# Performance work log

Measured on AMD Instinct MI355X. Metric: run time of the kernel, lower is better.

Reference implementation:

```python
import jax, jax.numpy as jnp
import numpy as np

STEPS = 100
VTH = 1.0
POOL_TH = 0.75


def _conv(x, w):
    # 5x5 conv, stride 1, pad 2, no bias; NCHW / OIHW
    return jax.lax.conv_general_dilated(
        x, w, window_strides=(1, 1), padding=[(2, 2), (2, 2)],
        dimension_numbers=('NCHW', 'OIHW', 'NCHW'))


def _avgpool2(x):
    s = jax.lax.reduce_window(x, 0.0, jax.lax.add, (1, 1, 2, 2), (1, 1, 2, 2), 'VALID')
    return s * 0.25


def _fire(mem, th):
    # torch.nn.functional.threshold(mem, th, 0): keep values > th, else 0
    ex = jnp.where(mem > th, mem, 0.0)
    mem = mem - ex
    out = (ex > 0).astype(mem.dtype)
    return mem, out


def _ave(output, inp):
    c = inp >= output
    denom = jnp.sum(jnp.where(c, inp, 0.0))
    num = jnp.sum(jnp.where(c, output, 0.0))
    return jnp.where(denom < 1e-3, 1.0, num / denom)


def _ave_p(output, inp):
    denom = jnp.sum(inp)
    return jnp.where(denom < 1e-3, 1.0, jnp.sum(output) / denom)


def setup_inputs() -> dict:
    key = jax.random.key(0)
    k_in, k1, k2, k3, k4 = jax.random.split(key, 5)
    B = 512
    inputdata = jax.random.uniform(k_in, (B, 1, 28, 28), dtype=jnp.float32)
    w1 = jax.random.normal(k1, (20, 1, 5, 5), dtype=jnp.float32) * np.sqrt(2.0 / (5 * 5 * 1))
    w2 = jax.random.normal(k2, (50, 20, 5, 5), dtype=jnp.float32) * np.sqrt(2.0 / (5 * 5 * 20))
    wf0 = jax.random.normal(k3, (200, 2450), dtype=jnp.float32) * np.sqrt(2.0 / 2450)
    wf1 = jax.random.normal(k4, (10, 200), dtype=jnp.float32) * np.sqrt(2.0 / 200)
    return {'inputdata': inputdata, 'w1': w1, 'w2': w2, 'wf0': wf0, 'wf1': wf1}


def _spiking_loop(inputdata, w1, w2, wf0, wf1):
    B = inputdata.shape[0]
    f32 = jnp.float32
    z = lambda *s: jnp.zeros(s, f32)
    carry0 = (
        z(B, 20, 28, 28), z(B, 20, 14, 14), z(B, 50, 14, 14), z(B, 50, 7, 7), z(B, 200),  # membranes
        z(B, 1, 28, 28),                                                                   # Total_input
        z(B, 20, 28, 28), z(B, 20, 28, 28),   # Total_1_output, IF_in_c1
        z(B, 20, 14, 14), z(B, 20, 14, 14),   # Total_p1_output, IF_in_p1
        z(B, 50, 14, 14), z(B, 50, 14, 14),   # Total_2_output, IF_in_c2
        z(B, 50, 7, 7), z(B, 50, 7, 7),       # Total_p2_output, IF_in_p2
        z(B, 200), z(B, 200),                  # Total_f0_output, IF_in_f0
    )

    sgn = jnp.sign(inputdata)
    half = jnp.abs(inputdata) / 2.0

    def step(carry, k):
        (m1, m1s, m2, m2s, mf0, Tin, T1, IFc1, Tp1, IFp1, T2, IFc2, Tp2, IFp2, Tf0, IFf0) = carry
        r = jax.random.uniform(k, inputdata.shape, dtype=f32)
        poisson = (half > r).astype(f32) * sgn
        Tin = Tin + poisson

        a = _conv(poisson, w1)
        m1 = m1 + a
        m1, o = _fire(m1, VTH)            # LIF (l=1 -> membrane unchanged)
        IFc1 = IFc1 + a
        T1 = T1 + o

        a = _avgpool2(o)
        m1s = m1s + a
        m1s, o = _fire(m1s, POOL_TH)
        IFp1 = IFp1 + a
        Tp1 = Tp1 + o

        a = _conv(o, w2)
        m2 = m2 + a
        m2, o = _fire(m2, VTH)
        IFc2 = IFc2 + a
        T2 = T2 + o

        a = _avgpool2(o)
        m2s = m2s + a
        m2s, o = _fire(m2s, POOL_TH)
        IFp2 = IFp2 + a
        Tp2 = Tp2 + o

        a = o.reshape(B, -1) @ wf0.T
        mf0 = mf0 + a
        mf0, o = _fire(mf0, VTH)
        IFf0 = IFf0 + a
        Tf0 = Tf0 + o

        return (m1, m1s, m2, m2s, mf0, Tin, T1, IFc1, Tp1, IFp1, T2, IFc2, Tp2, IFp2, Tf0, IFf0), None

    keys = jax.random.split(jax.random.key(42), STEPS)
    carry, _ = jax.lax.scan(step, carry0, keys)
    return jax.lax.stop_gradient(carry)  # loop ran under torch.no_grad()


def _forward(inputdata, w1, w2, wf0, wf1):
    sg = jax.lax.stop_gradient
    (_, _, _, _, _, Tin, T1, IFc1, Tp1, IFp1, T2, IFc2, Tp2, IFp2, Tf0, IFf0) = \
        _spiking_loop(inputdata, w1, w2, wf0, wf1)

    # global scales start at 1, sign == 1 branch taken
    s1 = 0.6 * _ave(T1, IFc1) + 0.4
    s2 = 0.6 * _ave_p(Tp1, IFp1) + 0.4
    s3 = 0.6 * _ave(T2, IFc2) + 0.4
    s4 = 0.6 * _ave_p(Tp2, IFp2) + 0.4
    s5 = 0.6 * _ave(Tf0, IFf0) + 0.4
    sc1 = s1 * (IFc1 > 0).astype(jnp.float32)
    sc2 = s2 * (IFp1 > 0).astype(jnp.float32)
    sc3 = s3 * (IFc2 > 0).astype(jnp.float32)
    sc4 = s4 * (IFp2 > 0).astype(jnp.float32)
    sc5 = s5 * (IFf0 > 0).astype(jnp.float32)

    # straight-through graph (ASF-BP)
    B = inputdata.shape[0]
    o = _conv(Tin, w1) * sc1
    T1g = o - sg(o) + T1
    o = _avgpool2(T1g) * sc2
    Tp1g = o - sg(o) + Tp1
    o = _conv(Tp1g, w2) * sc3
    T2g = o - sg(o) + T2
    o = _avgpool2(T2g) * sc4
    Tp2g = o - sg(o) + Tp2
    o = (Tp2g.reshape(B, -1) @ wf0.T) * sc5
    Tf0g = o - sg(o) + Tf0
    fc1_in = Tf0g @ wf1.T
    return fc1_in / VTH / STEPS


def reference(inputdata, w1, w2, wf0, wf1):
    return _forward(inputdata, w1, w2, wf0, wf1)
```

## Files before the change

kernel.cpp:

```cpp
#include <hip/hip_runtime.h>
#include <stdint.h>

#define STEPS 100

typedef float f2 __attribute__((ext_vector_type(2)));

__device__ __forceinline__ uint32_t rotl32(uint32_t v, int r) {
  return (v << r) | (v >> (32 - r));
}

__device__ __forceinline__ void tf2x32(uint32_t k0, uint32_t k1,
                                       uint32_t x0, uint32_t x1,
                                       uint32_t& o0, uint32_t& o1) {
  uint32_t ks2 = k0 ^ k1 ^ 0x1BD11BDAu;
  x0 += k0; x1 += k1;
#define RND(r) { x0 += x1; x1 = rotl32(x1, (r)); x1 ^= x0; }
  RND(13) RND(15) RND(26) RND(6)
  x0 += k1;  x1 += ks2 + 1u;
  RND(17) RND(29) RND(16) RND(24)
  x0 += ks2; x1 += k0 + 2u;
  RND(13) RND(15) RND(26) RND(6)
  x0 += k0;  x1 += k1 + 3u;
  RND(17) RND(29) RND(16) RND(24)
  x0 += k1;  x1 += ks2 + 4u;
  RND(13) RND(15) RND(26) RND(6)
  x0 += ks2; x1 += k0 + 5u;
#undef RND
  o0 = x0; o1 = x1;
}

__global__ void keys_k(uint32_t* __restrict__ kb) {
  int i = threadIdx.x;
  if (i < STEPS) {
    uint32_t a, b;
    tf2x32(0u, 42u, 0u, (uint32_t)i, a, b);
    kb[2 * i] = a;
    kb[2 * i + 1] = b;
  }
}

__global__ void wt3_k(const float* __restrict__ w2, float* __restrict__ wT3) {
  int i = blockIdx.x * blockDim.x + threadIdx.x;
  if (i >= 50 * 20 * 72) return;
  int oc = i / 1440, r = i % 1440;
  int ic = r / 72, q = r % 72;
  int jr = q / 12, p = q % 12;
  float v = 0.f;
  if (p < 10) {
    int kx = p >> 1, h = p & 1;
    if (h == 0 && jr < 5)  v = w2[oc * 500 + ic * 25 + jr * 5 + kx];
    if (h == 1 && jr >= 1) v = w2[oc * 500 + ic * 25 + (jr - 1) * 5 + kx];
  }
  wT3[i] = v;
}

__global__ void wf0t_k(const float* __restrict__ wf0,
                       float* __restrict__ wf0T) {
  int i = blockIdx.x * blockDim.x + threadIdx.x;
  if (i >= 2450 * 256) return;
  int k = i >> 8, n = i & 255;
  wf0T[i] = (n < 200) ? wf0[n * 2450 + k] : 0.f;
}

__device__ __forceinline__ void p2blk(const float4& q0, const float4& q1,
                                      const float4& q2, const float4& q3,
                                      const f2* wp, f2* acc2) {
  float u[18] = {q0.x, q0.y, q0.z, q0.w, q1.x, q1.y, q1.z, q1.w,
                 q2.x, q2.y, q2.z, q2.w, q3.x, q3.y, q3.z, q3.w, 0.f, 0.f};
#pragma unroll
  for (int kx = 0; kx < 5; ++kx) {
    f2 w = wp[kx];
#pragma unroll
    for (int xx = 0; xx < 14; ++xx) {
      f2 us = {u[xx + kx], u[xx + kx]};
      acc2[xx] = __builtin_elementwise_fma(w, us, acc2[xx]);
    }
  }
}

__device__ __forceinline__ void ldwp(const float* wic, int jr, f2* wp) {
  const float4* p = reinterpret_cast<const float4*>(wic + jr * 12);
  float4 a = p[0], b = p[1];
  float2 c = *reinterpret_cast<const float2*>(wic + jr * 12 + 8);
  wp[0] = f2{a.x, a.y}; wp[1] = f2{a.z, a.w};
  wp[2] = f2{b.x, b.y}; wp[3] = f2{b.z, b.w};
  wp[4] = f2{c.x, c.y};
}

__global__ __launch_bounds__(512, 2) void step_all_k(
    const float* __restrict__ x, const float* __restrict__ w1,
    const float* __restrict__ wT3, const uint32_t* __restrict__ kb,
    uint32_t* __restrict__ sp2g) {
  __shared__ __align__(16) float  xhs_l[784];
  __shared__ __align__(16) float  pois_l[32 * 34];
  __shared__ __align__(16) float  sp1_l[20 * 18 * 20];
  __shared__ int8_t s2_l[50 * 196];
  __shared__ __align__(16) float  m2_l[50 * 196];
  __shared__ float  m2s_l[2450];
  __shared__ float  m1s_l[20 * 196];
  __shared__ float  m1stash[512 * 21];

  const int b  = blockIdx.x;
  const int t  = threadIdx.x;
  const int lq = t & 255;
  const int ohu = __builtin_amdgcn_readfirstlane(t >> 8);
  const bool act1 = lq < 196;
  const int qy = lq / 14, qx = lq % 14;
  const bool act2 = t < 350;
  const int oc2 = t / 7;
  const int rp  = t % 7;
  const int y0  = 2 * rp;

  for (int p = t; p < 784; p += 512) {
    xhs_l[p] = x[b * 784 + p] * 0.5f;
  }
  for (int i = t; i < 32 * 34; i += 512) pois_l[i] = 0.f;
  for (int i = t; i < 20 * 360; i += 512) sp1_l[i] = 0.f;
  for (int i = t; i < 50 * 196; i += 512) m2_l[i] = 0.f;
  for (int i = t; i < 2450; i += 512) m2s_l[i] = 0.f;
  for (int i = t; i < 20 * 196; i += 512) m1s_l[i] = 0.f;
  for (int i = t; i < 512 * 21; i += 512) m1stash[i] = 0.f;

  float m1p[2][10];
#pragma unroll
  for (int i = 0; i < 10; ++i) {
    m1p[0][i] = 0.f;
    m1p[1][i] = 0.f;
  }
  __syncthreads();

  {
    uint32_t k0 = kb[0], k1 = kb[1];
    for (int p = t; p < 784; p += 512) {
      uint32_t o0, o1;
      tf2x32(k0, k1, 0u, (uint32_t)(b * 784 + p), o0, o1);
      float r = __uint_as_float(((o0 ^ o1) >> 9) | 0x3F800000u) - 1.0f;
      float v = xhs_l[p];
      pois_l[(p / 28 + 2) * 34 + (p % 28 + 2)] =
          (fabsf(v) > r) ? ((v > 0.f) ? 1.f : -1.f) : 0.f;
    }
  }
  __syncthreads();

#define LDROW(rr, d) {                                                      \
    const float2* _pr = reinterpret_cast<const float2*>(                    \
        &pois_l[(2 * qy + (rr)) * 34 + 2 * qx]);                            \
    float2 _a0 = _pr[0], _a1 = _pr[1], _a2 = _pr[2];                        \
    d[0] = _a0.x; d[1] = _a0.y; d[2] = _a1.x;                               \
    d[3] = _a1.y; d[4] = _a2.x; d[5] = _a2.y; }

#define LD4(base, p0, p1, p2, p3) {                                         \
    const float4* _rn = reinterpret_cast<const float4*>(base);              \
    p0 = _rn[0]; p1 = _rn[1]; p2 = _rn[2]; p3 = _rn[3]; }

  for (int s = 0; s < STEPS; ++s) {
    if (act1) {
      float rA[6], rB[6];
      LDROW(0, rA)
      LDROW(1, rB)
      float acc[4][10];
#pragma unroll
      for (int tt = 0; tt < 4; ++tt)
#pragma unroll
        for (int i = 0; i < 10; ++i) acc[tt][i] = 0.f;
#pragma unroll
      for (int ky = 0; ky < 5; ++ky) {
#pragma unroll
        for (int kx = 0; kx < 5; ++kx) {
#pragma unroll
          for (int i = 0; i < 10; ++i) {
            float w = w1[(ohu * 10 + i) * 25 + ky * 5 + kx];
            acc[0][i] += w * rA[kx];
            acc[1][i] += w * rA[kx + 1];
            acc[2][i] += w * rB[kx];
            acc[3][i] += w * rB[kx + 1];
          }
        }
        if (ky < 4) {
#pragma unroll
          for (int j = 0; j < 6; ++j) rA[j] = rB[j];
          LDROW(ky + 2, rB)
        }
      }
#pragma unroll
      for (int i = 0; i < 10; ++i) {
        float s4[4];
#pragma unroll
        for (int tt = 0; tt < 2; ++tt) {
          float m = m1p[tt][i] + acc[tt][i];
          float sp = 0.f;
          if (m > 1.0f) { sp = 1.f; m = 0.f; }
          m1p[tt][i] = m;
          s4[tt] = sp;
        }
        {
          float m = m1stash[t * 21 + i] + acc[2][i];
          float sp = 0.f;
          if (m > 1.0f) { sp = 1.f; m = 0.f; }
          m1stash[t * 21 + i] = m;
          s4[2] = sp;
        }
        {
          float m = m1stash[t * 21 + 10 + i] + acc[3][i];
          float sp = 0.f;
          if (m > 1.0f) { sp = 1.f; m = 0.f; }
          m1stash[t * 21 + 10 + i] = m;
          s4[3] = sp;
        }
        float a = 0.25f * (((s4[0] + s4[1]) + s4[2]) + s4[3]);
        int mi = (ohu * 10 + i) * 196 + lq;
        float mm = m1s_l[mi] + a;
        float spp = 0.f;
        if (mm > 0.75f) { spp = 1.f; mm = 0.f; }
        m1s_l[mi] = mm;
        sp1_l[(ohu * 10 + i) * 360 + (qy + 2) * 20 + (qx + 2)] = spp;
      }
    }
    __syncthreads();

    if (act2) {
      f2 acc2[14];
#pragma unroll
      for (int xx = 0; xx < 14; ++xx) acc2[xx] = f2{0.f, 0.f};
      const float* wb = wT3 + oc2 * 1440;
#pragma unroll 1
      for (int ic = 0; ic < 20; ++ic) {
        const float* wic = wb + ic * 72;
        const float* spi = sp1_l + ic * 360;
        float4 a0, a1, a2, a3, b0, b1, b2, b3;
        f2 wpA[5], wpB[5];
        LD4(spi + (y0 + 0) * 20, a0, a1, a2, a3)
        ldwp(wic, 0, wpA);
        LD4(spi + (y0 + 1) * 20, b0, b1, b2, b3)
        ldwp(wic, 1, wpB);
        p2blk(a0, a1, a2, a3, wpA, acc2);
        LD4(spi + (y0 + 2) * 20, a0, a1, a2, a3)
        ldwp(wic, 2, wpA);
        __builtin_amdgcn_sched_barrier(0);
        p2blk(b0, b1, b2, b3, wpB, acc2);
        LD4(spi + (y0 + 3) * 20, b0, b1, b2, b3)
        ldwp(wic, 3, wpB);
        __builtin_amdgcn_sched_barrier(0);
        p2blk(a0, a1, a2, a3, wpA, acc2);
        LD4(spi + (y0 + 4) * 20, a0, a1, a2, a3)
        ldwp(wic, 4, wpA);
        __builtin_amdgcn_sched_barrier(0);
        p2blk(b0, b1, b2, b3, wpB, acc2);
        LD4(spi + (y0 + 5) * 20, b0, b1, b2, b3)
        ldwp(wic, 5, wpB);
        __builtin_amdgcn_sched_barrier(0);
        p2blk(a0, a1, a2, a3, wpA, acc2);
        p2blk(b0, b1, b2, b3, wpB, acc2);
      }
#pragma unroll
      for (int xx = 0; xx < 14; ++xx) {
        int li = oc2 * 196 + y0 * 14 + xx;
        float m = m2_l[li] + acc2[xx].x;
        int8_t sp = 0;
        if (m > 1.0f) { sp = 1; m = 0.f; }
        m2_l[li] = m;
        s2_l[li] = sp;
      }
#pragma unroll
      for (int xx = 0; xx < 14; ++xx) {
        int li = oc2 * 196 + (y0 + 1) * 14 + xx;
        float m = m2_l[li] + acc2[xx].y;
        int8_t sp = 0;
        if (m > 1.0f) { sp = 1; m = 0.f; }
        m2_l[li] = m;
        s2_l[li] = sp;
      }
    }
    __syncthreads();

#pragma unroll
    for (int i = 0; i < 5; ++i) {
      int e = i * 512 + t;
      bool fire = false;
      if (e < 2450) {
        int oc = e / 49, qq = e % 49;
        int yo = qq / 7, xo = qq % 7;
        int ib = oc * 196 + 2 * yo * 14 + 2 * xo;
        float s00 = (float)s2_l[ib];
        float s01 = (float)s2_l[ib + 1];
        float s10 = (float)s2_l[ib + 14];
        float s11 = (float)s2_l[ib + 15];
        float a = 0.25f * (((s00 + s01) + s10) + s11);
        float m = m2s_l[e] + a;
        if (m > 0.75f) { fire = true; m = 0.f; }
        m2s_l[e] = m;
      }
      unsigned long long mask = __ballot(fire);
      int base = (e & ~63);
      if ((t & 63) == 0 && base < 2450) {
        int d = base >> 5;
        sp2g[b * 7700 + s * 77 + d] = (uint32_t)mask;
        if (base + 32 < 2450)
          sp2g[b * 7700 + s * 77 + d + 1] = (uint32_t)(mask >> 32);
      }
    }
    if (s + 1 < STEPS) {
      uint32_t k0 = kb[2 * (s + 1)], k1 = kb[2 * (s + 1) + 1];
      for (int p = t; p < 784; p += 512) {
        uint32_t o0, o1;
        tf2x32(k0, k1, 0u, (uint32_t)(b * 784 + p), o0, o1);
        float r = __uint_as_float(((o0 ^ o1) >> 9) | 0x3F800000u) - 1.0f;
        float v = xhs_l[p];
        pois_l[(p / 28 + 2) * 34 + (p % 28 + 2)] =
            (fabsf(v) > r) ? ((v > 0.f) ? 1.f : -1.f) : 0.f;
      }
    }
    __syncthreads();
  }
#undef LDROW
#undef LD4
}

__global__ __launch_bounds__(256) void fc0f_k(
    const uint32_t* __restrict__ sp2g, const float* __restrict__ wf0T,
    float* __restrict__ Tf0g) {
  __shared__ uint32_t mk[77];
  const int b = blockIdx.x;
  const int n = threadIdx.x;
  float m = 0.f, T = 0.f;
  for (int s = 0; s < STEPS; ++s) {
    __syncthreads();
    if (n < 77) mk[n] = sp2g[b * 7700 + s * 77 + n];
    __syncthreads();
    float acc = 0.f;
    for (int d = 0; d < 77; ++d) {
      uint32_t um = mk[d];
      while (um) {
        int j = __builtin_ctz(um);
        um &= um - 1;
        acc += wf0T[((d << 5) + j) * 256 + n];
      }
    }
    m += acc;
    if (m > 1.0f) { T += 1.f; m = 0.f; }
  }
  if (n < 200) Tf0g[b * 200 + n] = T;
}

__global__ void fc1_k(const float* __restrict__ Tf0,
                      const float* __restrict__ wf1,
                      float* __restrict__ out) {
  int idx = blockIdx.x * blockDim.x + threadIdx.x;
  if (idx >= 5120) return;
  int b = idx / 10, i = idx % 10;
  float a = 0.f;
  for (int j = 0; j < 200; ++j) a += Tf0[b * 200 + j] * wf1[i * 200 + j];
  out[idx] = (a / 1.0f) / 100.0f;
}

extern "C" void kernel_launch(void* const* d_in, const int* in_sizes, int n_in,
                              void* d_out, int out_size, void* d_ws, size_t ws_size,
                              hipStream_t stream) {
  (void)in_sizes; (void)n_in; (void)out_size; (void)ws_size;
  const float* x   = (const float*)d_in[0];
  const float* w1  = (const float*)d_in[1];
  const float* w2  = (const float*)d_in[2];
  const float* wf0 = (const float*)d_in[3];
  const float* wf1 = (const float*)d_in[4];
  float* out = (float*)d_out;
  char* ws = (char*)d_ws;

  const size_t tf0_b  = 512ull * 200 * 4;
  const size_t wt_b   = 50ull * 20 * 72 * 4;
  const size_t key_b  = 1024;
  const size_t wf0t_b = 2450ull * 256 * 4;
  float*    Tf0g = (float*)ws;
  float*    wT3  = (float*)(ws + tf0_b);
  uint32_t* kb   = (uint32_t*)(ws + tf0_b + wt_b);
  float*    wf0T = (float*)(ws + tf0_b + wt_b + key_b);
  uint32_t* sp2g = (uint32_t*)(ws + tf0_b + wt_b + key_b + wf0t_b);

  keys_k<<<1, 128, 0, stream>>>(kb);
  wt3_k<<<282, 256, 0, stream>>>(w2, wT3);
  wf0t_k<<<2450, 256, 0, stream>>>(wf0, wf0T);
  step_all_k<<<512, 512, 0, stream>>>(x, w1, wT3, kb, sp2g);
  fc0f_k<<<512, 256, 0, stream>>>(sp2g, wf0T, Tf0g);
  fc1_k<<<20, 256, 0, stream>>>(Tf0g, wf1, out);
}
```

Measured before the change: 10.38 ms.

## Fuse pool2 into conv2 threads, pipeline conv2 loads, overlap RNG on idle threads

Each conv2 thread now average-pools its own 2x14 output strip into the second pooled membrane and packs the 7 spike bits into a shared byte. This removes the int8 spike buffer, the separate pooling pass, and one block-wide barrier per step. Threads 0-76 then gather those bytes into 32-bit words for the global spike mask. The conv2 input-channel loop is software-pipelined, prefetching rows and weights for the next channel across iterations. Poisson generation for the next step moves onto the otherwise idle threads 384-511 so it overlaps with conv2, at the cost of fewer threads doing that RNG work and more complex bit-packing logic.

```diff
diff --git a/kernel.cpp b/kernel.cpp
--- a/kernel.cpp
+++ b/kernel.cpp
@@ -81,9 +81,9 @@
 __device__ __forceinline__ void ldwp(const float* wic, int jr, f2* wp) {
   const float4* p = reinterpret_cast<const float4*>(wic + jr * 12);
   float4 a = p[0], b = p[1];
-  float2 c = *reinterpret_cast<const float2*>(wic + jr * 12 + 8);
   wp[0] = f2{a.x, a.y}; wp[1] = f2{a.z, a.w};
   wp[2] = f2{b.x, b.y}; wp[3] = f2{b.z, b.w};
+  float2 c = *reinterpret_cast<const float2*>(wic + jr * 12 + 8);
   wp[4] = f2{c.x, c.y};
 }
 
@@ -94,11 +94,11 @@
   __shared__ __align__(16) float  xhs_l[784];
   __shared__ __align__(16) float  pois_l[32 * 34];
   __shared__ __align__(16) float  sp1_l[20 * 18 * 20];
-  __shared__ int8_t s2_l[50 * 196];
   __shared__ __align__(16) float  m2_l[50 * 196];
-  __shared__ float  m2s_l[2450];
-  __shared__ float  m1s_l[20 * 196];
-  __shared__ float  m1stash[512 * 21];
+  __shared__ float    m2s_l[2450];
+  __shared__ float    m1s_l[20 * 196];
+  __shared__ float    m1stash[512 * 21];
+  __shared__ uint8_t  fb[352];
 
   const int b  = blockIdx.x;
   const int t  = threadIdx.x;
@@ -120,6 +120,7 @@
   for (int i = t; i < 2450; i += 512) m2s_l[i] = 0.f;
   for (int i = t; i < 20 * 196; i += 512) m1s_l[i] = 0.f;
   for (int i = t; i < 512 * 21; i += 512) m1stash[i] = 0.f;
+  if (t < 352) fb[t] = 0;
 
   float m1p[2][10];
 #pragma unroll
@@ -149,8 +150,9 @@
     d[0] = _a0.x; d[1] = _a0.y; d[2] = _a1.x;                               \
     d[3] = _a1.y; d[4] = _a2.x; d[5] = _a2.y; }
 
-#define LD4(base, p0, p1, p2, p3) {                                         \
-    const float4* _rn = reinterpret_cast<const float4*>(base);              \
+#define LD4(icv, jrv, p0, p1, p2, p3) {                                     \
+    const float4* _rn = reinterpret_cast<const float4*>(                    \
+        sp1_l + (icv) * 360 + (y0 + (jrv)) * 20);                           \
     p0 = _rn[0]; p1 = _rn[1]; p2 = _rn[2]; p3 = _rn[3]; }
 
   for (int s = 0; s < STEPS; ++s) {
@@ -223,94 +225,101 @@
 #pragma unroll
       for (int xx = 0; xx < 14; ++xx) acc2[xx] = f2{0.f, 0.f};
       const float* wb = wT3 + oc2 * 1440;
+      float4 A0, A1, A2, A3, B0, B1, B2, B3;
+      f2 W0[5], W1[5], W2[5];
+      LD4(0, 0, A0, A1, A2, A3)
+      ldwp(wb, 0, W0);
+      LD4(0, 1, B0, B1, B2, B3)
+      ldwp(wb, 1, W1);
+      ldwp(wb, 2, W2);
 #pragma unroll 1
       for (int ic = 0; ic < 20; ++ic) {
-        const float* wic = wb + ic * 72;
-        const float* spi = sp1_l + ic * 360;
-        float4 a0, a1, a2, a3, b0, b1, b2, b3;
-        f2 wpA[5], wpB[5];
-        LD4(spi + (y0 + 0) * 20, a0, a1, a2, a3)
-        ldwp(wic, 0, wpA);
-        LD4(spi + (y0 + 1) * 20, b0, b1, b2, b3)
-        ldwp(wic, 1, wpB);
-        p2blk(a0, a1, a2, a3, wpA, acc2);
-        LD4(spi + (y0 + 2) * 20, a0, a1, a2, a3)
-        ldwp(wic, 2, wpA);
-        __builtin_amdgcn_sched_barrier(0);
-        p2blk(b0, b1, b2, b3, wpB, acc2);
-        LD4(spi + (y0 + 3) * 20, b0, b1, b2, b3)
-        ldwp(wic, 3, wpB);
-        __builtin_amdgcn_sched_barrier(0);
-        p2blk(a0, a1, a2, a3, wpA, acc2);
-        LD4(spi + (y0 + 4) * 20, a0, a1, a2, a3)
-        ldwp(wic, 4, wpA);
-        __builtin_amdgcn_sched_barrier(0);
-        p2blk(b0, b1, b2, b3, wpB, acc2);
-        LD4(spi + (y0 + 5) * 20, b0, b1, b2, b3)
-        ldwp(wic, 5, wpB);
-        __builtin_amdgcn_sched_barrier(0);
-        p2blk(a0, a1, a2, a3, wpA, acc2);
-        p2blk(b0, b1, b2, b3, wpB, acc2);
-      }
+        const int icn = (ic < 19) ? ic + 1 : 19;
+        const float* wic  = wb + ic * 72;
+        const float* wicn = wb + icn * 72;
+        p2blk(A0, A1, A2, A3, W0, acc2);
+        LD4(ic, 2, A0, A1, A2, A3)
+        ldwp(wic, 3, W0);
+        __builtin_amdgcn_sched_barrier(0);
+        p2blk(B0, B1, B2, B3, W1, acc2);
+        LD4(ic, 3, B0, B1, B2, B3)
+        ldwp(wic, 4, W1);
+        __builtin_amdgcn_sched_barrier(0);
+        p2blk(A0, A1, A2, A3, W2, acc2);
+        LD4(ic, 4, A0, A1, A2, A3)
+        ldwp(wic, 5, W2);
+        __builtin_amdgcn_sched_barrier(0);
+        p2blk(B0, B1, B2, B3, W0, acc2);
+        LD4(ic, 5, B0, B1, B2, B3)
+        ldwp(wicn, 0, W0);
+        __builtin_amdgcn_sched_barrier(0);
+        p2blk(A0, A1, A2, A3, W1, acc2);
+        LD4(icn, 0, A0, A1, A2, A3)
+        ldwp(wicn, 1, W1);
+        __builtin_amdgcn_sched_barrier(0);
+        p2blk(B0, B1, B2, B3, W2, acc2);
+        LD4(icn, 1, B0, B1, B2, B3)
+        ldwp(wicn, 2, W2);
+        __builtin_amdgcn_sched_barrier(0);
+      }
+      float f0[14], f1[14];
 #pragma unroll
       for (int xx = 0; xx < 14; ++xx) {
         int li = oc2 * 196 + y0 * 14 + xx;
         float m = m2_l[li] + acc2[xx].x;
-        int8_t sp = 0;
-        if (m > 1.0f) { sp = 1; m = 0.f; }
+        float sp = 0.f;
+        if (m > 1.0f) { sp = 1.f; m = 0.f; }
         m2_l[li] = m;
-        s2_l[li] = sp;
+        f0[xx] = sp;
       }
 #pragma unroll
       for (int xx = 0; xx < 14; ++xx) {
         int li = oc2 * 196 + (y0 + 1) * 14 + xx;
         float m = m2_l[li] + acc2[xx].y;
-        int8_t sp = 0;
-        if (m > 1.0f) { sp = 1; m = 0.f; }
+        float sp = 0.f;
+        if (m > 1.0f) { sp = 1.f; m = 0.f; }
         m2_l[li] = m;
-        s2_l[li] = sp;
+        f1[xx] = sp;
+      }
+      uint32_t byte = 0;
+#pragma unroll
+      for (int xo = 0; xo < 7; ++xo) {
+        float a = 0.25f * (((f0[2 * xo] + f0[2 * xo + 1]) + f1[2 * xo]) +
+                           f1[2 * xo + 1]);
+        int e = oc2 * 49 + rp * 7 + xo;
+        float m = m2s_l[e] + a;
+        uint32_t bit = 0;
+        if (m > 0.75f) { bit = 1; m = 0.f; }
+        m2s_l[e] = m;
+        byte |= bit << xo;
+      }
+      fb[t] = (uint8_t)byte;
+    } else if (t >= 384) {
+      if (s + 1 < STEPS) {
+        uint32_t k0 = kb[2 * (s + 1)], k1 = kb[2 * (s + 1) + 1];
+        for (int p = t - 384; p < 784; p += 128) {
+          uint32_t o0, o1;
+          tf2x32(k0, k1, 0u, (uint32_t)(b * 784 + p), o0, o1);
+          float r = __uint_as_float(((o0 ^ o1) >> 9) | 0x3F800000u) - 1.0f;
+          float v = xhs_l[p];
+          pois_l[(p / 28 + 2) * 34 + (p % 28 + 2)] =
+              (fabsf(v) > r) ? ((v > 0.f) ? 1.f : -1.f) : 0.f;
+        }
       }
     }
     __syncthreads();
 
-#pragma unroll
-    for (int i = 0; i < 5; ++i) {
-      int e = i * 512 + t;
-      bool fire = false;
-      if (e < 2450) {
-        int oc = e / 49, qq = e % 49;
-        int yo = qq / 7, xo = qq % 7;
-        int ib = oc * 196 + 2 * yo * 14 + 2 * xo;
-        float s00 = (float)s2_l[ib];
-        float s01 = (float)s2_l[ib + 1];
-        float s10 = (float)s2_l[ib + 14];
-        float s11 = (float)s2_l[ib + 15];
-        float a = 0.25f * (((s00 + s01) + s10) + s11);
-        float m = m2s_l[e] + a;
-        if (m > 0.75f) { fire = true; m = 0.f; }
-        m2s_l[e] = m;
-      }
-      unsigned long long mask = __ballot(fire);
-      int base = (e & ~63);
-      if ((t & 63) == 0 && base < 2450) {
-        int d = base >> 5;
-        sp2g[b * 7700 + s * 77 + d] = (uint32_t)mask;
-        if (base + 32 < 2450)
-          sp2g[b * 7700 + s * 77 + d + 1] = (uint32_t)(mask >> 32);
-      }
-    }
-    if (s + 1 < STEPS) {
-      uint32_t k0 = kb[2 * (s + 1)], k1 = kb[2 * (s + 1) + 1];
-      for (int p = t; p < 784; p += 512) {
-        uint32_t o0, o1;
-        tf2x32(k0, k1, 0u, (uint32_t)(b * 784 + p), o0, o1);
-        float r = __uint_as_float(((o0 ^ o1) >> 9) | 0x3F800000u) - 1.0f;
-        float v = xhs_l[p];
-        pois_l[(p / 28 + 2) * 34 + (p % 28 + 2)] =
-            (fabsf(v) > r) ? ((v > 0.f) ? 1.f : -1.f) : 0.f;
-      }
-    }
-    __syncthreads();
+    if (t < 77) {
+      int j0 = (32 * t) / 7;
+      uint64_t accw = 0;
+#pragma unroll
+      for (int jj = 0; jj < 6; ++jj) {
+        int j = j0 + jj;
+        uint32_t bv = (j < 350) ? (uint32_t)fb[j] : 0u;
+        accw |= (uint64_t)bv << (7 * j - 32 * t + 6);
+      }
+      sp2g[b * 7700 + s * 77 + t] = (uint32_t)(accw >> 6);
+    }
   }
 #undef LDROW
 #undef LD4
```

After: 9.912 ms. 4.5% less time.
